# Performance work log

Measured on AMD Instinct MI355X. Metric: run time of the kernel, lower is better.

## Reference

```python
import jax, jax.numpy as jnp
import numpy as np

D_MODEL = 1024
NUM_HEADS = 16
HEAD_DIM = D_MODEL // NUM_HEADS


def setup_inputs() -> dict:
    key = jax.random.key(0)
    ks = jax.random.split(key, 5)
    x = jax.random.normal(ks[0], (2, 2048, D_MODEL), dtype=jnp.float32)
    # torch.nn.Linear default init ~ U(-1/sqrt(fan_in), 1/sqrt(fan_in)); scale roughly
    s = 1.0 / np.sqrt(D_MODEL)
    W_qkv = jax.random.uniform(ks[1], (D_MODEL, 3 * D_MODEL), jnp.float32, -s, s)
    b_qkv = jax.random.uniform(ks[2], (3 * D_MODEL,), jnp.float32, -s, s)
    W_out = jax.random.uniform(ks[3], (D_MODEL, D_MODEL), jnp.float32, -s, s)
    b_out = jax.random.uniform(ks[4], (D_MODEL,), jnp.float32, -s, s)
    return {"x": x, "W_qkv": W_qkv, "b_qkv": b_qkv, "W_out": W_out, "b_out": b_out}


def reference(x, W_qkv, b_qkv, W_out, b_out):
    B, S, D = x.shape
    H, Hd = NUM_HEADS, HEAD_DIM
    qkv = x @ W_qkv + b_qkv                      # [B,S,3D]
    q, k, v = jnp.split(qkv, 3, axis=-1)
    def split_heads(t):
        return t.reshape(B, S, H, Hd).transpose(0, 2, 1, 3)  # [B,H,S,Hd]
    q, k, v = split_heads(q), split_heads(k), split_heads(v)
    scores = jnp.einsum('bhqd,bhkd->bhqk', q, k) / jnp.sqrt(jnp.float32(Hd))
    weights = jax.nn.softmax(scores, axis=-1)
    attn = jnp.einsum('bhqk,bhkd->bhqd', weights, v)
    attn = attn.transpose(0, 2, 1, 3).reshape(B, S, D)
    return attn @ W_out + b_out
```

## Files before the change

### kernel.cpp

```cpp
#include <hip/hip_runtime.h>
#include <hip/hip_bf16.h>

#define DMODEL 1024
#define NH 16
#define HD 64
#define SEQ 2048
#define BATCH 2
#define BH (BATCH * NH)
#define MTOT (BATCH * SEQ)

typedef _Float16 f16x8 __attribute__((ext_vector_type(8)));
typedef float f32x4 __attribute__((ext_vector_type(4)));

__device__ __forceinline__ void gload_lds16(const void* g, void* l) {
  __builtin_amdgcn_global_load_lds((const __attribute__((address_space(1))) unsigned*)g,
                                   (__attribute__((address_space(3))) unsigned*)l, 16, 0, 0);
}

__global__ __launch_bounds__(256) void cvt_f2h(const float* __restrict__ in,
                                               _Float16* __restrict__ out, int n8) {
  const int i = blockIdx.x * 256 + threadIdx.x;
  if (i < n8) {
    const float4 a = ((const float4*)in)[i * 2];
    const float4 b = ((const float4*)in)[i * 2 + 1];
    f16x8 o = {(_Float16)a.x, (_Float16)a.y, (_Float16)a.z, (_Float16)a.w,
               (_Float16)b.x, (_Float16)b.y, (_Float16)b.z, (_Float16)b.w};
    *(f16x8*)&out[(size_t)i * 8] = o;
  }
}

__global__ __launch_bounds__(256) void cvt_transpose(const float* __restrict__ W,
                                                     _Float16* __restrict__ Wt,
                                                     int N, int K) {
  __shared__ float Ls[64][65];
  const int k0 = blockIdx.y * 64, n0 = blockIdx.x * 64;
  const int t = threadIdx.x;
  const int r = t >> 2, c4 = (t & 3) * 16;
#pragma unroll
  for (int j = 0; j < 4; ++j) {
    const float4 v = *(const float4*)&W[(size_t)(k0 + r) * N + n0 + c4 + j * 4];
    Ls[r][c4 + j * 4 + 0] = v.x;
    Ls[r][c4 + j * 4 + 1] = v.y;
    Ls[r][c4 + j * 4 + 2] = v.z;
    Ls[r][c4 + j * 4 + 3] = v.w;
  }
  __syncthreads();
  f16x8 o0, o1;
#pragma unroll
  for (int j = 0; j < 8; ++j) {
    o0[j] = (_Float16)Ls[c4 + j][r];
    o1[j] = (_Float16)Ls[c4 + 8 + j][r];
  }
  *(f16x8*)&Wt[(size_t)(n0 + r) * K + k0 + c4] = o0;
  *(f16x8*)&Wt[(size_t)(n0 + r) * K + k0 + c4 + 8] = o1;
}

__global__ __launch_bounds__(256) void qkv_mm(const _Float16* __restrict__ A,
                                              const _Float16* __restrict__ Bt,
                                              const float* __restrict__ bias,
                                              _Float16* __restrict__ qh,
                                              _Float16* __restrict__ kh,
                                              _Float16* __restrict__ vh) {
  __shared__ __align__(16) _Float16 As[128 * 64];
  __shared__ __align__(16) _Float16 Bs[128 * 64];
  const int t = threadIdx.x;
  const int w = t >> 6, lane = t & 63;
  const int g = lane >> 4, lr = lane & 15;
  const int m0 = blockIdx.y * 128, n0 = blockIdx.x * 128;
  const int wr = w >> 1, wc = w & 1;
  const int srow = (lane >> 3);
  const int col8 = (lane & 7) * 8;
  f32x4 acc[4][4] = {};

  for (int k0 = 0; k0 < DMODEL; k0 += 64) {
    __syncthreads();
#pragma unroll
    for (int i = 0; i < 4; ++i) {
      const int row = w * 32 + i * 8 + srow;
      gload_lds16(A + (size_t)(m0 + row) * DMODEL + k0 + col8, &As[(w * 4 + i) * 512]);
      gload_lds16(Bt + (size_t)(n0 + row) * DMODEL + k0 + col8, &Bs[(w * 4 + i) * 512]);
    }
    __syncthreads();
#pragma unroll
    for (int ks = 0; ks < 2; ++ks) {
      f16x8 af[4], bf[4];
#pragma unroll
      for (int mi = 0; mi < 4; ++mi)
        af[mi] = *(const f16x8*)&As[(wr * 64 + mi * 16 + lr) * 64 + ks * 32 + g * 8];
#pragma unroll
      for (int ni = 0; ni < 4; ++ni)
        bf[ni] = *(const f16x8*)&Bs[(wc * 64 + ni * 16 + lr) * 64 + ks * 32 + g * 8];
#pragma unroll
      for (int mi = 0; mi < 4; ++mi)
#pragma unroll
        for (int ni = 0; ni < 4; ++ni)
          acc[mi][ni] = __builtin_amdgcn_mfma_f32_16x16x32_f16(af[mi], bf[ni], acc[mi][ni], 0, 0, 0);
    }
  }

#pragma unroll
  for (int ni = 0; ni < 4; ++ni) {
    const int n = n0 + wc * 64 + ni * 16 + lr;
    const float bn = bias[n];
    const int which = n >> 10, d = n & 1023, h = d >> 6, hd = d & 63;
    _Float16* dst = which == 0 ? qh : which == 1 ? kh : vh;
    const float scale = which == 0 ? 0.125f : 1.0f;
#pragma unroll
    for (int mi = 0; mi < 4; ++mi)
#pragma unroll
      for (int r = 0; r < 4; ++r) {
        const int m = m0 + wr * 64 + mi * 16 + g * 4 + r;
        const int bb = m >> 11, ss = m & 2047;
        dst[((size_t)(bb * NH + h) * SEQ + ss) * HD + hd] =
            (_Float16)((acc[mi][ni][r] + bn) * scale);
      }
  }
}

__global__ __launch_bounds__(256) void attn_fused(const _Float16* __restrict__ qh,
                                                  const _Float16* __restrict__ kh,
                                                  const _Float16* __restrict__ vh,
                                                  _Float16* __restrict__ ao) {
  __shared__ __align__(16) _Float16 Vt[64][72];
  __shared__ __align__(16) _Float16 Ps[4][16][72];
  const int t = threadIdx.x;
  const int lane = t & 63, w = t >> 6;
  const int g = lane >> 4, lr = lane & 15;
  const int bh = blockIdx.y, qt = blockIdx.x;
  const _Float16* Qp = qh + (size_t)bh * SEQ * HD;
  const _Float16* Kp = kh + (size_t)bh * SEQ * HD;
  const _Float16* Vp = vh + (size_t)bh * SEQ * HD;
  const int q0 = qt * 64 + w * 16;

  const f16x8 aq0 = *reinterpret_cast<const f16x8*>(Qp + (size_t)(q0 + lr) * HD + g * 8);
  const f16x8 aq1 = *reinterpret_cast<const f16x8*>(Qp + (size_t)(q0 + lr) * HD + 32 + g * 8);

  f32x4 o[4] = {};
  float mrun[4], lrun[4];
#pragma unroll
  for (int r = 0; r < 4; ++r) { mrun[r] = -1e30f; lrun[r] = 0.f; }

  const int stV_kv = t >> 2;
  const int stV_d0 = (t & 3) * 16;

  for (int kv0 = 0; kv0 < SEQ; kv0 += 64) {
    const f16x8 v0 = *reinterpret_cast<const f16x8*>(Vp + (size_t)(kv0 + stV_kv) * HD + stV_d0);
    const f16x8 v1 = *reinterpret_cast<const f16x8*>(Vp + (size_t)(kv0 + stV_kv) * HD + stV_d0 + 8);
#pragma unroll
    for (int e = 0; e < 8; ++e) {
      Vt[stV_d0 + e][stV_kv] = v0[e];
      Vt[stV_d0 + 8 + e][stV_kv] = v1[e];
    }

    f32x4 s[4];
#pragma unroll
    for (int cb = 0; cb < 4; ++cb) {
      const f16x8 bk0 =
          *reinterpret_cast<const f16x8*>(Kp + (size_t)(kv0 + cb * 16 + lr) * HD + g * 8);
      const f16x8 bk1 =
          *reinterpret_cast<const f16x8*>(Kp + (size_t)(kv0 + cb * 16 + lr) * HD + 32 + g * 8);
      f32x4 z = {};
      z = __builtin_amdgcn_mfma_f32_16x16x32_f16(aq0, bk0, z, 0, 0, 0);
      z = __builtin_amdgcn_mfma_f32_16x16x32_f16(aq1, bk1, z, 0, 0, 0);
      s[cb] = z;
    }

    float mx[4];
#pragma unroll
    for (int r = 0; r < 4; ++r)
      mx[r] = fmaxf(fmaxf(s[0][r], s[1][r]), fmaxf(s[2][r], s[3][r]));
#pragma unroll
    for (int off = 1; off <= 8; off <<= 1)
#pragma unroll
      for (int r = 0; r < 4; ++r) mx[r] = fmaxf(mx[r], __shfl_xor(mx[r], off, 64));

    float p[4][4];
    float corr[4], rsum[4];
#pragma unroll
    for (int r = 0; r < 4; ++r) {
      const float mnew = fmaxf(mrun[r], mx[r]);
      corr[r] = __expf(mrun[r] - mnew);
      mrun[r] = mnew;
      float sum = 0.f;
#pragma unroll
      for (int cb = 0; cb < 4; ++cb) {
        p[cb][r] = __expf(s[cb][r] - mnew);
        sum += p[cb][r];
      }
      rsum[r] = sum;
    }
#pragma unroll
    for (int off = 1; off <= 8; off <<= 1)
#pragma unroll
      for (int r = 0; r < 4; ++r) rsum[r] += __shfl_xor(rsum[r], off, 64);
#pragma unroll
    for (int r = 0; r < 4; ++r) lrun[r] = lrun[r] * corr[r] + rsum[r];
#pragma unroll
    for (int dcb = 0; dcb < 4; ++dcb)
#pragma unroll
      for (int r = 0; r < 4; ++r) o[dcb][r] *= corr[r];

#pragma unroll
    for (int cb = 0; cb < 4; ++cb)
#pragma unroll
      for (int r = 0; r < 4; ++r) Ps[w][g * 4 + r][cb * 16 + lr] = (_Float16)p[cb][r];

    __syncthreads();

    const f16x8 pa0 = *reinterpret_cast<const f16x8*>(&Ps[w][lr][g * 8]);
    const f16x8 pa1 = *reinterpret_cast<const f16x8*>(&Ps[w][lr][32 + g * 8]);
#pragma unroll
    for (int dcb = 0; dcb < 4; ++dcb) {
      const f16x8 bv0 = *reinterpret_cast<const f16x8*>(&Vt[dcb * 16 + lr][g * 8]);
      const f16x8 bv1 = *reinterpret_cast<const f16x8*>(&Vt[dcb * 16 + lr][32 + g * 8]);
      o[dcb] = __builtin_amdgcn_mfma_f32_16x16x32_f16(pa0, bv0, o[dcb], 0, 0, 0);
      o[dcb] = __builtin_amdgcn_mfma_f32_16x16x32_f16(pa1, bv1, o[dcb], 0, 0, 0);
    }
    __syncthreads();
  }

  _Float16* aob = ao + (size_t)bh * SEQ * HD;
#pragma unroll
  for (int r = 0; r < 4; ++r) {
    const float inv = 1.0f / lrun[r];
#pragma unroll
    for (int dcb = 0; dcb < 4; ++dcb)
      aob[(size_t)(q0 + g * 4 + r) * HD + dcb * 16 + lr] = (_Float16)(o[dcb][r] * inv);
  }
}

__global__ __launch_bounds__(256) void out_mm(const _Float16* __restrict__ Ah,
                                              const _Float16* __restrict__ Bt,
                                              const float* __restrict__ bias,
                                              float* __restrict__ out) {
  __shared__ __align__(16) _Float16 As[128 * 64];
  __shared__ __align__(16) _Float16 Bs[128 * 64];
  const int t = threadIdx.x;
  const int w = t >> 6, lane = t & 63;
  const int g = lane >> 4, lr = lane & 15;
  const int m0 = blockIdx.y * 128, n0 = blockIdx.x * 128;
  const int wr = w >> 1, wc = w & 1;
  const int srow = (lane >> 3);
  const int col8 = (lane & 7) * 8;
  f32x4 acc[4][4] = {};

  for (int k0 = 0; k0 < DMODEL; k0 += 64) {
    const int h = k0 >> 6;
    __syncthreads();
#pragma unroll
    for (int i = 0; i < 4; ++i) {
      const int row = w * 32 + i * 8 + srow;
      const int m = m0 + row;
      const int bb = m >> 11, ss = m & 2047;
      gload_lds16(Ah + ((size_t)(bb * NH + h) * SEQ + ss) * HD + col8, &As[(w * 4 + i) * 512]);
      gload_lds16(Bt + (size_t)(n0 + row) * DMODEL + k0 + col8, &Bs[(w * 4 + i) * 512]);
    }
    __syncthreads();
#pragma unroll
    for (int ks = 0; ks < 2; ++ks) {
      f16x8 af[4], bf[4];
#pragma unroll
      for (int mi = 0; mi < 4; ++mi)
        af[mi] = *(const f16x8*)&As[(wr * 64 + mi * 16 + lr) * 64 + ks * 32 + g * 8];
#pragma unroll
      for (int ni = 0; ni < 4; ++ni)
        bf[ni] = *(const f16x8*)&Bs[(wc * 64 + ni * 16 + lr) * 64 + ks * 32 + g * 8];
#pragma unroll
      for (int mi = 0; mi < 4; ++mi)
#pragma unroll
        for (int ni = 0; ni < 4; ++ni)
          acc[mi][ni] = __builtin_amdgcn_mfma_f32_16x16x32_f16(af[mi], bf[ni], acc[mi][ni], 0, 0, 0);
    }
  }

#pragma unroll
  for (int ni = 0; ni < 4; ++ni) {
    const int n = n0 + wc * 64 + ni * 16 + lr;
    const float bn = bias[n];
#pragma unroll
    for (int mi = 0; mi < 4; ++mi)
#pragma unroll
      for (int r = 0; r < 4; ++r) {
        const int m = m0 + wr * 64 + mi * 16 + g * 4 + r;
        out[(size_t)m * DMODEL + n] = acc[mi][ni][r] + bn;
      }
  }
}

extern "C" void kernel_launch(void* const* d_in, const int* in_sizes, int n_in,
                              void* d_out, int out_size, void* d_ws, size_t ws_size,
                              hipStream_t stream) {
  const float* x = (const float*)d_in[0];
  const float* Wqkv = (const float*)d_in[1];
  const float* bqkv = (const float*)d_in[2];
  const float* Wout = (const float*)d_in[3];
  const float* bout = (const float*)d_in[4];
  float* out = (float*)d_out;

  char* ws = (char*)d_ws;
  const size_t MB = 1u << 20;
  _Float16* Xh = (_Float16*)(ws);
  _Float16* qh = (_Float16*)(ws + 8 * MB);
  _Float16* kh = (_Float16*)(ws + 16 * MB);
  _Float16* vh = (_Float16*)(ws + 24 * MB);
  _Float16* Wtq = (_Float16*)(ws + 32 * MB);
  _Float16* Wto = (_Float16*)(ws + 38 * MB + 512 * 1024);
  _Float16* attnh = Xh;

  cvt_f2h<<<dim3(MTOT * DMODEL / 8 / 256), 256, 0, stream>>>(x, Xh, MTOT * DMODEL / 8);
  cvt_transpose<<<dim3(3072 / 64, DMODEL / 64), 256, 0, stream>>>(Wqkv, Wtq, 3072, DMODEL);
  cvt_transpose<<<dim3(DMODEL / 64, DMODEL / 64), 256, 0, stream>>>(Wout, Wto, DMODEL, DMODEL);
  qkv_mm<<<dim3(3072 / 128, MTOT / 128), 256, 0, stream>>>(Xh, Wtq, bqkv, qh, kh, vh);
  attn_fused<<<dim3(SEQ / 64, BH), 256, 0, stream>>>(qh, kh, vh, attnh);
  out_mm<<<dim3(DMODEL / 128, MTOT / 128), 256, 0, stream>>>(attnh, Wto, bout, out);
}
```

Baseline: 306.7 us.

## Rewrite attention with transposed 32x32x16 MFMA and register-resident P

Reworks the attention kernel so each wave owns 32 queries and computes S^T = K·Q^T with 32x32x16 MFMA, so every lane holds one query column. The row max and sum then reduce mostly within registers plus a single cross-half shuffle. P is repacked to fp16 through a lane shuffle instead of round-tripping through shared memory, and the query tile per block doubles to 128. This is meant to cut LDS traffic, shuffle reductions and one barrier per step, at the cost of higher register pressure (launch bounds 256,2) and half as many blocks.

Result: faster. 253.9 us (-17.2%).

```diff
diff --git a/kernel.cpp b/kernel.cpp
--- a/kernel.cpp
+++ b/kernel.cpp
@@ -10,7 +10,10 @@
 #define MTOT (BATCH * SEQ)
 
 typedef _Float16 f16x8 __attribute__((ext_vector_type(8)));
+typedef _Float16 f16x4 __attribute__((ext_vector_type(4)));
+typedef _Float16 f16x2 __attribute__((ext_vector_type(2)));
 typedef float f32x4 __attribute__((ext_vector_type(4)));
+typedef float f32x16 __attribute__((ext_vector_type(16)));
 
 __device__ __forceinline__ void gload_lds16(const void* g, void* l) {
   __builtin_amdgcn_global_load_lds((const __attribute__((address_space(1))) unsigned*)g,
@@ -117,115 +120,131 @@
   }
 }
 
-__global__ __launch_bounds__(256) void attn_fused(const _Float16* __restrict__ qh,
-                                                  const _Float16* __restrict__ kh,
-                                                  const _Float16* __restrict__ vh,
-                                                  _Float16* __restrict__ ao) {
-  __shared__ __align__(16) _Float16 Vt[64][72];
-  __shared__ __align__(16) _Float16 Ps[4][16][72];
+__global__ __launch_bounds__(256, 2) void attn_fused(const _Float16* __restrict__ qh,
+                                                     const _Float16* __restrict__ kh,
+                                                     const _Float16* __restrict__ vh,
+                                                     _Float16* __restrict__ ao) {
+  __shared__ __align__(16) _Float16 Vt[64][76];
   const int t = threadIdx.x;
   const int lane = t & 63, w = t >> 6;
-  const int g = lane >> 4, lr = lane & 15;
-  const int bh = blockIdx.y, qt = blockIdx.x;
+  const int q = lane & 31, hi = lane >> 5;
+  const int bh = blockIdx.y;
+  const int q0 = blockIdx.x * 128 + w * 32;
   const _Float16* Qp = qh + (size_t)bh * SEQ * HD;
   const _Float16* Kp = kh + (size_t)bh * SEQ * HD;
   const _Float16* Vp = vh + (size_t)bh * SEQ * HD;
-  const int q0 = qt * 64 + w * 16;
-
-  const f16x8 aq0 = *reinterpret_cast<const f16x8*>(Qp + (size_t)(q0 + lr) * HD + g * 8);
-  const f16x8 aq1 = *reinterpret_cast<const f16x8*>(Qp + (size_t)(q0 + lr) * HD + 32 + g * 8);
-
-  f32x4 o[4] = {};
-  float mrun[4], lrun[4];
-#pragma unroll
-  for (int r = 0; r < 4; ++r) { mrun[r] = -1e30f; lrun[r] = 0.f; }
-
-  const int stV_kv = t >> 2;
-  const int stV_d0 = (t & 3) * 16;
+
+  f16x8 qf[4];
+#pragma unroll
+  for (int ks = 0; ks < 4; ++ks)
+    qf[ks] = *(const f16x8*)(Qp + (size_t)(q0 + q) * HD + ks * 16 + hi * 8);
+
+  f32x16 o0 = {}, o1 = {};
+  float mrun = -3e30f, lrun = 0.f;
+
+  const int skv = t & 63;
+  const int sq4 = t >> 6;
 
   for (int kv0 = 0; kv0 < SEQ; kv0 += 64) {
-    const f16x8 v0 = *reinterpret_cast<const f16x8*>(Vp + (size_t)(kv0 + stV_kv) * HD + stV_d0);
-    const f16x8 v1 = *reinterpret_cast<const f16x8*>(Vp + (size_t)(kv0 + stV_kv) * HD + stV_d0 + 8);
+    const f16x8 sv0 = *(const f16x8*)(Vp + (size_t)(kv0 + skv) * HD + sq4 * 16);
+    const f16x8 sv1 = *(const f16x8*)(Vp + (size_t)(kv0 + skv) * HD + sq4 * 16 + 8);
+    __syncthreads();
 #pragma unroll
     for (int e = 0; e < 8; ++e) {
-      Vt[stV_d0 + e][stV_kv] = v0[e];
-      Vt[stV_d0 + 8 + e][stV_kv] = v1[e];
-    }
-
-    f32x4 s[4];
-#pragma unroll
-    for (int cb = 0; cb < 4; ++cb) {
-      const f16x8 bk0 =
-          *reinterpret_cast<const f16x8*>(Kp + (size_t)(kv0 + cb * 16 + lr) * HD + g * 8);
-      const f16x8 bk1 =
-          *reinterpret_cast<const f16x8*>(Kp + (size_t)(kv0 + cb * 16 + lr) * HD + 32 + g * 8);
-      f32x4 z = {};
-      z = __builtin_amdgcn_mfma_f32_16x16x32_f16(aq0, bk0, z, 0, 0, 0);
-      z = __builtin_amdgcn_mfma_f32_16x16x32_f16(aq1, bk1, z, 0, 0, 0);
-      s[cb] = z;
-    }
-
-    float mx[4];
-#pragma unroll
-    for (int r = 0; r < 4; ++r)
-      mx[r] = fmaxf(fmaxf(s[0][r], s[1][r]), fmaxf(s[2][r], s[3][r]));
-#pragma unroll
-    for (int off = 1; off <= 8; off <<= 1)
-#pragma unroll
-      for (int r = 0; r < 4; ++r) mx[r] = fmaxf(mx[r], __shfl_xor(mx[r], off, 64));
-
-    float p[4][4];
-    float corr[4], rsum[4];
-#pragma unroll
-    for (int r = 0; r < 4; ++r) {
-      const float mnew = fmaxf(mrun[r], mx[r]);
-      corr[r] = __expf(mrun[r] - mnew);
-      mrun[r] = mnew;
-      float sum = 0.f;
-#pragma unroll
-      for (int cb = 0; cb < 4; ++cb) {
-        p[cb][r] = __expf(s[cb][r] - mnew);
-        sum += p[cb][r];
+      Vt[sq4 * 16 + e][skv] = sv0[e];
+      Vt[sq4 * 16 + 8 + e][skv] = sv1[e];
+    }
+
+    f32x16 s0 = {}, s1 = {};
+#pragma unroll
+    for (int ks = 0; ks < 4; ++ks) {
+      const f16x8 k0 = *(const f16x8*)(Kp + (size_t)(kv0 + q) * HD + ks * 16 + hi * 8);
+      const f16x8 k1 = *(const f16x8*)(Kp + (size_t)(kv0 + 32 + q) * HD + ks * 16 + hi * 8);
+      s0 = __builtin_amdgcn_mfma_f32_32x32x16_f16(k0, qf[ks], s0, 0, 0, 0);
+      s1 = __builtin_amdgcn_mfma_f32_32x32x16_f16(k1, qf[ks], s1, 0, 0, 0);
+    }
+
+    float tm[16];
+#pragma unroll
+    for (int r = 0; r < 16; ++r) tm[r] = fmaxf(s0[r], s1[r]);
+#pragma unroll
+    for (int d = 8; d > 0; d >>= 1)
+#pragma unroll
+      for (int r = 0; r < d; ++r) tm[r] = fmaxf(tm[r], tm[r + d]);
+    float mx = fmaxf(tm[0], __shfl_xor(tm[0], 32));
+    const float mnew = fmaxf(mrun, mx);
+    const float corr = __expf(mrun - mnew);
+    mrun = mnew;
+#pragma unroll
+    for (int r = 0; r < 16; ++r) {
+      s0[r] = __expf(s0[r] - mnew);
+      s1[r] = __expf(s1[r] - mnew);
+    }
+    float ts[16];
+#pragma unroll
+    for (int r = 0; r < 16; ++r) ts[r] = s0[r] + s1[r];
+#pragma unroll
+    for (int d = 8; d > 0; d >>= 1)
+#pragma unroll
+      for (int r = 0; r < d; ++r) ts[r] += ts[r + d];
+    float rs = ts[0] + __shfl_xor(ts[0], 32);
+    lrun = lrun * corr + rs;
+#pragma unroll
+    for (int r = 0; r < 16; ++r) {
+      o0[r] *= corr;
+      o1[r] *= corr;
+    }
+
+    __syncthreads();
+
+#pragma unroll
+    for (int ks = 0; ks < 4; ++ks) {
+      const int base = 8 * (ks & 1);
+      unsigned u0, u1, u2, u3;
+#pragma unroll
+      for (int w01 = 0; w01 < 2; ++w01) {
+        float a0, a1, b0, b1;
+        if (ks < 2) {
+          a0 = s0[base + 2 * w01];     a1 = s0[base + 2 * w01 + 1];
+          b0 = s0[base + 4 + 2 * w01]; b1 = s0[base + 4 + 2 * w01 + 1];
+        } else {
+          a0 = s1[base + 2 * w01];     a1 = s1[base + 2 * w01 + 1];
+          b0 = s1[base + 4 + 2 * w01]; b1 = s1[base + 4 + 2 * w01 + 1];
+        }
+        f16x2 hm0; hm0[0] = (_Float16)a0; hm0[1] = (_Float16)a1;
+        f16x2 hm1; hm1[0] = (_Float16)b0; hm1[1] = (_Float16)b1;
+        unsigned Pm0, Pm1;
+        __builtin_memcpy(&Pm0, &hm0, 4);
+        __builtin_memcpy(&Pm1, &hm1, 4);
+        const unsigned local = hi ? Pm1 : Pm0;
+        const unsigned sent = hi ? Pm0 : Pm1;
+        const unsigned cross = __shfl_xor(sent, 32);
+        const unsigned wa = hi ? cross : local;
+        const unsigned wb = hi ? local : cross;
+        if (w01 == 0) { u0 = wa; u2 = wb; } else { u1 = wa; u3 = wb; }
       }
-      rsum[r] = sum;
-    }
-#pragma unroll
-    for (int off = 1; off <= 8; off <<= 1)
-#pragma unroll
-      for (int r = 0; r < 4; ++r) rsum[r] += __shfl_xor(rsum[r], off, 64);
-#pragma unroll
-    for (int r = 0; r < 4; ++r) lrun[r] = lrun[r] * corr[r] + rsum[r];
-#pragma unroll
-    for (int dcb = 0; dcb < 4; ++dcb)
-#pragma unroll
-      for (int r = 0; r < 4; ++r) o[dcb][r] *= corr[r];
-
-#pragma unroll
-    for (int cb = 0; cb < 4; ++cb)
-#pragma unroll
-      for (int r = 0; r < 4; ++r) Ps[w][g * 4 + r][cb * 16 + lr] = (_Float16)p[cb][r];
-
-    __syncthreads();
-
-    const f16x8 pa0 = *reinterpret_cast<const f16x8*>(&Ps[w][lr][g * 8]);
-    const f16x8 pa1 = *reinterpret_cast<const f16x8*>(&Ps[w][lr][32 + g * 8]);
-#pragma unroll
-    for (int dcb = 0; dcb < 4; ++dcb) {
-      const f16x8 bv0 = *reinterpret_cast<const f16x8*>(&Vt[dcb * 16 + lr][g * 8]);
-      const f16x8 bv1 = *reinterpret_cast<const f16x8*>(&Vt[dcb * 16 + lr][32 + g * 8]);
-      o[dcb] = __builtin_amdgcn_mfma_f32_16x16x32_f16(pa0, bv0, o[dcb], 0, 0, 0);
-      o[dcb] = __builtin_amdgcn_mfma_f32_16x16x32_f16(pa1, bv1, o[dcb], 0, 0, 0);
-    }
-    __syncthreads();
-  }
-
-  _Float16* aob = ao + (size_t)bh * SEQ * HD;
-#pragma unroll
-  for (int r = 0; r < 4; ++r) {
-    const float inv = 1.0f / lrun[r];
-#pragma unroll
-    for (int dcb = 0; dcb < 4; ++dcb)
-      aob[(size_t)(q0 + g * 4 + r) * HD + dcb * 16 + lr] = (_Float16)(o[dcb][r] * inv);
+      unsigned ww[4] = {u0, u1, u2, u3};
+      f16x8 pb;
+      __builtin_memcpy(&pb, ww, 16);
+      const f16x8 va0 = *(const f16x8*)&Vt[0 + q][ks * 16 + hi * 8];
+      const f16x8 va1 = *(const f16x8*)&Vt[32 + q][ks * 16 + hi * 8];
+      o0 = __builtin_amdgcn_mfma_f32_32x32x16_f16(va0, pb, o0, 0, 0, 0);
+      o1 = __builtin_amdgcn_mfma_f32_32x32x16_f16(va1, pb, o1, 0, 0, 0);
+    }
+  }
+
+  const float invl = 1.0f / lrun;
+  _Float16* aob = ao + (size_t)bh * SEQ * HD + (size_t)(q0 + q) * HD;
+#pragma unroll
+  for (int m = 0; m < 4; ++m) {
+    f16x4 v0, v1;
+#pragma unroll
+    for (int s2 = 0; s2 < 4; ++s2) {
+      v0[s2] = (_Float16)(o0[4 * m + s2] * invl);
+      v1[s2] = (_Float16)(o1[4 * m + s2] * invl);
+    }
+    *(f16x4*)(aob + 8 * m + 4 * hi) = v0;
+    *(f16x4*)(aob + 32 + 8 * m + 4 * hi) = v1;
   }
 }
 
@@ -311,6 +330,6 @@
   cvt_transpose<<<dim3(3072 / 64, DMODEL / 64), 256, 0, stream>>>(Wqkv, Wtq, 3072, DMODEL);
   cvt_transpose<<<dim3(DMODEL / 64, DMODEL / 64), 256, 0, stream>>>(Wout, Wto, DMODEL, DMODEL);
   qkv_mm<<<dim3(3072 / 128, MTOT / 128), 256, 0, stream>>>(Xh, Wtq, bqkv, qh, kh, vh);
-  attn_fused<<<dim3(SEQ / 64, BH), 256, 0, stream>>>(qh, kh, vh, attnh);
+  attn_fused<<<dim3(SEQ / 128, BH), 256, 0, stream>>>(qh, kh, vh, attnh);
   out_mm<<<dim3(DMODEL / 128, MTOT / 128), 256, 0, stream>>>(attnh, Wto, bout, out);
 }
```
